# Kernel tuning notes

Measured on AMD Instinct MI355X. Metric: run time of the kernel, lower is better.

The kernel has to match this reference:

```python
import jax, jax.numpy as jnp
import numpy as np

B, N, D = 4, 4096, 1024
LN_EPS = 1e-5

def setup_inputs() -> dict:
    key = jax.random.key(0)
    ks = jax.random.split(key, 12)
    s = 1.0 / np.sqrt(D)
    return {
        "embeddings": jax.random.normal(ks[0], (B, N, D), dtype=jnp.float32),
        "edge_indices": jax.random.randint(ks[1], (2, 8192), 0, N, dtype=jnp.int64),
        "edge_times": jax.random.uniform(ks[2], (8192,), dtype=jnp.float32),
        "timestamps": jax.random.uniform(ks[3], (N,), dtype=jnp.float32),
        "Wq": jax.random.uniform(ks[4], (D, D), jnp.float32, -s, s),
        "bq": jax.random.uniform(ks[5], (D,), jnp.float32, -s, s),
        "Wk": jax.random.uniform(ks[6], (D, D), jnp.float32, -s, s),
        "bk": jax.random.uniform(ks[7], (D,), jnp.float32, -s, s),
        "Wv": jax.random.uniform(ks[8], (D, D), jnp.float32, -s, s),
        "bv": jax.random.uniform(ks[9], (D,), jnp.float32, -s, s),
        "gamma": jnp.ones((D,), jnp.float32),
        "beta": jnp.zeros((D,), jnp.float32),
    }

def reference(embeddings, edge_indices, edge_times, timestamps,
              Wq, bq, Wk, bk, Wv, bv, gamma, beta):
    # edge_indices / edge_times / timestamps are unused by the original forward.
    d = embeddings.shape[-1]
    q = jnp.einsum("bnd,ed->bne", embeddings, Wq) + bq   # [B,N,D]
    k = jnp.einsum("bnd,ed->bne", embeddings, Wk) + bk
    v = jnp.einsum("bnd,ed->bne", embeddings, Wv) + bv
    scores = jnp.einsum("bnd,bmd->bnm", q, k) / jnp.sqrt(jnp.asarray(d, embeddings.dtype))
    attn = jax.nn.softmax(scores, axis=-1)                # [B,N,N]
    attended = jnp.einsum("bnm,bmd->bnd", attn, v)
    x = embeddings + attended
    mu = jnp.mean(x, axis=-1, keepdims=True)
    var = jnp.mean(jnp.square(x - mu), axis=-1, keepdims=True)
    return gamma * (x - mu) * jax.lax.rsqrt(var + LN_EPS) + beta
```

## Files before the change

### kernel.cpp

```cpp
#include <hip/hip_runtime.h>
#include <hip/hip_fp8.h>

typedef unsigned short u16;
typedef unsigned char  u8;
typedef long long      i64;
using bf16x8 = __attribute__((ext_vector_type(8))) __bf16;
using f32x4  = __attribute__((ext_vector_type(4))) float;

__device__ __forceinline__ u16 f2bf(float f) {
    unsigned u = __builtin_bit_cast(unsigned, f);
    u += 0x7fffu + ((u >> 16) & 1u);
    return (u16)(u >> 16);
}
__device__ __forceinline__ float bf2f(u16 h) {
    unsigned u = ((unsigned)h) << 16;
    return __builtin_bit_cast(float, u);
}
__device__ __forceinline__ u8 f2fp8(float f) {
    __hip_fp8_e4m3 t(f);
    return t.__x;
}
__device__ __forceinline__ float wred_sum(float v) {
    #pragma unroll
    for (int o = 32; o; o >>= 1) v += __shfl_xor(v, o, 64);
    return v;
}

__device__ __forceinline__ void gl2lds16(const void* g, void* l) {
    __builtin_amdgcn_global_load_lds(
        (__attribute__((address_space(1))) void*)(g),
        (__attribute__((address_space(3))) void*)(l), 16, 0, 0);
}

__global__ __launch_bounds__(256)
void cast_bf16(const float* __restrict__ src, u16* __restrict__ dst, int n4) {
    int i = blockIdx.x * 256 + threadIdx.x;
    if (i < n4) {
        float4 f = ((const float4*)src)[i];
        ushort4 u;
        u.x = f2bf(f.x); u.y = f2bf(f.y); u.z = f2bf(f.z); u.w = f2bf(f.w);
        ((ushort4*)dst)[i] = u;
    }
}

template<int MODE>
__global__ __launch_bounds__(512, 2)
void gemm256(const u16* __restrict__ A, const u16* __restrict__ Bt,
             u16* __restrict__ oQ, u16* __restrict__ oK,
             const float* __restrict__ bQ, const float* __restrict__ bK,
             const float* __restrict__ bV,
             u8* __restrict__ oP, u8* __restrict__ oP2,
             float* __restrict__ sums, const float scale)
{
    __shared__ u16 smem[65536];
    const int tid = threadIdx.x;
    const int wv = tid >> 6, lane = tid & 63;
    const int wm = wv >> 2, wn = wv & 3;
    const int row0 = blockIdx.x << 8, col0 = blockIdx.y << 8;

    const size_t boff = (size_t)blockIdx.z * 4194304;
    const int srow = tid >> 2;
    const int scol = ((tid & 3) ^ ((tid >> 3) & 3)) << 3;
    const u16* gA = A + boff + (size_t)(row0 + srow) * 1024 + scol;
    const u16* gB = Bt + boff + (size_t)(col0 + srow) * 1024 + scol;
    char* lds = (char*)smem;
    const int wvo = wv << 10;

    const int fr = lane & 15, g = lane >> 4;
    const int kc = (g ^ ((fr >> 1) & 3)) << 4;

    f32x4 acc[8][4];
    #pragma unroll
    for (int i = 0; i < 8; i++)
        #pragma unroll
        for (int j = 0; j < 4; j++) acc[i][j] = (f32x4){0.f, 0.f, 0.f, 0.f};

    #define SG_A(ts, sl) { \
        gl2lds16(gA + (ts) * 32,          lds + (sl) * 32768 + wvo); \
        gl2lds16(gA + 131072 + (ts) * 32, lds + (sl) * 32768 + 8192 + wvo); }
    #define SG_B(ts, sl) { \
        gl2lds16(gB + (ts) * 32,          lds + (sl) * 32768 + 16384 + wvo); \
        gl2lds16(gB + 131072 + (ts) * 32, lds + (sl) * 32768 + 24576 + wvo); }

    SG_A(0, 0); SG_B(0, 0);
    SG_A(1, 1); SG_B(1, 1);
    SG_A(2, 2); SG_B(2, 2);
    asm volatile("s_waitcnt vmcnt(8)" ::: "memory");
    __builtin_amdgcn_s_barrier();

    for (int t = 0; t < 32; ++t) {
        const int slot = t & 3;
        const int ts = (t + 3) & 31;
        const int ns = (t + 3) & 3;
        const char* Ab = lds + slot * 32768;
        const char* Bb = Ab + 16384;

        SG_A(ts, ns);
        bf16x8 bf[4], af[4];
        #pragma unroll
        for (int j = 0; j < 4; ++j)
            bf[j] = *(const bf16x8*)(Bb + (wn * 64 + 16 * j + fr) * 64 + kc);
        #pragma unroll
        for (int i = 0; i < 4; ++i)
            af[i] = *(const bf16x8*)(Ab + (wm * 128 + 16 * i + fr) * 64 + kc);
        __builtin_amdgcn_sched_barrier(0);
        __builtin_amdgcn_s_barrier();
        asm volatile("s_waitcnt lgkmcnt(0)" ::: "memory");
        __builtin_amdgcn_sched_barrier(0);
        __builtin_amdgcn_s_setprio(1);
        #pragma unroll
        for (int i = 0; i < 4; ++i)
            #pragma unroll
            for (int j = 0; j < 4; ++j)
                acc[i][j] = __builtin_amdgcn_mfma_f32_16x16x32_bf16(af[i], bf[j], acc[i][j], 0, 0, 0);
        __builtin_amdgcn_s_setprio(0);

        SG_B(ts, ns);
        bf16x8 af2[4];
        #pragma unroll
        for (int i = 0; i < 4; ++i)
            af2[i] = *(const bf16x8*)(Ab + (wm * 128 + 64 + 16 * i + fr) * 64 + kc);
        asm volatile("s_waitcnt vmcnt(8)" ::: "memory");
        __builtin_amdgcn_sched_barrier(0);
        __builtin_amdgcn_s_barrier();
        asm volatile("s_waitcnt lgkmcnt(0)" ::: "memory");
        __builtin_amdgcn_sched_barrier(0);
        __builtin_amdgcn_s_setprio(1);
        #pragma unroll
        for (int i = 0; i < 4; ++i)
            #pragma unroll
            for (int j = 0; j < 4; ++j)
                acc[i + 4][j] = __builtin_amdgcn_mfma_f32_16x16x32_bf16(af2[i], bf[j], acc[i + 4][j], 0, 0, 0);
        __builtin_amdgcn_s_setprio(0);
    }
    #undef SG_A
    #undef SG_B

    asm volatile("s_waitcnt vmcnt(0)" ::: "memory");

    const int rB = (lane >> 4) << 2, cB = lane & 15;

    if (MODE == 0) {
        const int sel = col0 >> 10;
        if (sel < 2) {
            const float* bias = (sel == 0) ? bQ : bK;
            u16* dst = (sel == 0) ? oQ : oK;
            #pragma unroll
            for (int i = 0; i < 8; i++) {
                #pragma unroll
                for (int j = 0; j < 4; j++) {
                    const int m0 = row0 + wm * 128 + 16 * i + rB;
                    const int e  = (col0 & 1023) + wn * 64 + 16 * j + cB;
                    const float bb = bias[e];
                    #pragma unroll
                    for (int t = 0; t < 4; t++)
                        dst[(size_t)(m0 + t) * 1024 + e] = f2bf(acc[i][j][t] + bb);
                }
            }
        } else {
            const int b      = row0 >> 12;
            const int n_base = row0 & 4095;
            const int e0     = col0 & 1023;
            unsigned* lds32 = (unsigned*)smem;
            __syncthreads();
            #pragma unroll
            for (int i = 0; i < 8; i++) {
                const int n_l0 = wm * 128 + 16 * i + rB;
                const int gq   = n_l0 >> 4;
                const int kq   = (n_l0 >> 2) & 3;
                #pragma unroll
                for (int j = 0; j < 4; j++) {
                    const int e_p = wn * 64 + 16 * j + cB;
                    const float bb = bV[e0 + e_p];
                    union { u8 c[4]; unsigned u; } pk;
                    pk.c[0] = f2fp8(acc[i][j][0] + bb);
                    pk.c[1] = f2fp8(acc[i][j][1] + bb);
                    pk.c[2] = f2fp8(acc[i][j][2] + bb);
                    pk.c[3] = f2fp8(acc[i][j][3] + bb);
                    lds32[e_p * 64 + ((gq ^ (e_p & 15)) << 2) + kq] = pk.u;
                }
            }
            __syncthreads();
            #pragma unroll
            for (int it = 0; it < 8; ++it) {
                const int idx = it * 512 + tid;
                const int er  = idx >> 4;
                const int c16 = idx & 15;
                int4 v = *(const int4*)&lds32[er * 64 + ((c16 ^ (er & 15)) << 2)];
                *(int4*)&oP[(size_t)b * 4194304 +
                            (size_t)(e0 + er) * 4096 + n_base + c16 * 16] = v;
            }
        }
    } else {
        u8* Pz = blockIdx.z ? oP2 : oP;
        float* smz = sums + (blockIdx.z << 12);
        float psum[8][4];
        #pragma unroll
        for (int i = 0; i < 8; i++)
            #pragma unroll
            for (int t = 0; t < 4; t++) psum[i][t] = 0.f;

        #pragma unroll
        for (int i = 0; i < 8; i++) {
            const int m0 = row0 + wm * 128 + 16 * i + rB;
            #pragma unroll
            for (int j = 0; j < 4; j++) {
                const int c = col0 + wn * 64 + 16 * j + cB;
                #pragma unroll
                for (int t = 0; t < 4; t++) {
                    const float e = __expf(acc[i][j][t] * scale);
                    psum[i][t] += e;
                    Pz[(size_t)(m0 + t) * 4096 + c] = f2fp8(e);
                }
            }
        }
        #pragma unroll
        for (int i = 0; i < 8; i++) {
            #pragma unroll
            for (int t = 0; t < 4; t++) {
                float v = psum[i][t];
                v += __shfl_xor(v, 1, 64);
                v += __shfl_xor(v, 2, 64);
                v += __shfl_xor(v, 4, 64);
                v += __shfl_xor(v, 8, 64);
                if (cB == 0)
                    atomicAdd(&smz[row0 + wm * 128 + 16 * i + rB + t], v);
            }
        }
    }
}

__global__ __launch_bounds__(512, 2)
void pv256(const u8* __restrict__ p0, const u8* __restrict__ p1,
           const u8* __restrict__ p2, const u8* __restrict__ p3,
           const u8* __restrict__ vt8, const float* __restrict__ sums,
           float* __restrict__ out)
{
    __shared__ u8 smem[131072];
    const int b = blockIdx.z;
    const u8* Pb = (b == 0) ? p0 : (b == 1) ? p1 : (b == 2) ? p2 : p3;
    const u8* Vb = vt8 + (size_t)b * 4194304;
    const float* sm = sums + (b << 12);
    float* Ob = out + (size_t)b * 4194304;

    const int tid = threadIdx.x;
    const int wv = tid >> 6, lane = tid & 63;
    const int wm = wv >> 2, wn = wv & 3;
    const int row0 = blockIdx.x << 8, col0 = blockIdx.y << 8;

    const int srow = tid >> 2;
    const int sc16 = ((tid & 3) ^ ((tid >> 3) & 3)) << 4;
    const u8* gA = Pb + (size_t)(row0 + srow) * 4096 + sc16;
    const u8* gB = Vb + (size_t)(col0 + srow) * 4096 + sc16;
    char* lds = (char*)smem;
    const int wvo = wv << 10;

    const int fr = lane & 15, g = lane >> 4;
    const int sw = (fr >> 1) & 3;
    const int g2 = g >> 1, h8 = (g & 1) << 3;
    const int pc0 = ((g2 ^ sw) << 4) + h8;
    const int pc1 = (((2 + g2) ^ sw) << 4) + h8;

    f32x4 acc[8][4];
    #pragma unroll
    for (int i = 0; i < 8; i++)
        #pragma unroll
        for (int j = 0; j < 4; j++) acc[i][j] = (f32x4){0.f, 0.f, 0.f, 0.f};

    #define PG_A(ts, sl) { \
        gl2lds16(gA + (ts) * 64,          lds + (sl) * 32768 + wvo); \
        gl2lds16(gA + 524288 + (ts) * 64, lds + (sl) * 32768 + 8192 + wvo); }
    #define PG_B(ts, sl) { \
        gl2lds16(gB + (ts) * 64,          lds + (sl) * 32768 + 16384 + wvo); \
        gl2lds16(gB + 524288 + (ts) * 64, lds + (sl) * 32768 + 24576 + wvo); }

    PG_A(0, 0); PG_B(0, 0);
    PG_A(1, 1); PG_B(1, 1);
    PG_A(2, 2); PG_B(2, 2);
    asm volatile("s_waitcnt vmcnt(8)" ::: "memory");
    __builtin_amdgcn_s_barrier();

    for (int t = 0; t < 64; ++t) {
        const int slot = t & 3;
        const int ts = (t + 3) & 63;
        const int ns = (t + 3) & 3;
        const char* Ab = lds + slot * 32768;
        const char* Bb = Ab + 16384;

        PG_A(ts, ns);
        i64 af[8], bf[4];
        #pragma unroll
        for (int i = 0; i < 8; ++i) af[i] = *(const i64*)(Ab + (wm * 128 + 16 * i + fr) * 64 + pc0);
        #pragma unroll
        for (int j = 0; j < 4; ++j) bf[j] = *(const i64*)(Bb + (wn * 64 + 16 * j + fr) * 64 + pc0);
        __builtin_amdgcn_sched_barrier(0);
        __builtin_amdgcn_s_barrier();
        asm volatile("s_waitcnt lgkmcnt(0)" ::: "memory");
        __builtin_amdgcn_sched_barrier(0);
        __builtin_amdgcn_s_setprio(1);
        #pragma unroll
        for (int i = 0; i < 8; ++i)
            #pragma unroll
            for (int j = 0; j < 4; ++j)
                acc[i][j] = __builtin_amdgcn_mfma_f32_16x16x32_fp8_fp8(af[i], bf[j], acc[i][j], 0, 0, 0);
        __builtin_amdgcn_s_setprio(0);

        PG_B(ts, ns);
        #pragma unroll
        for (int i = 0; i < 8; ++i) af[i] = *(const i64*)(Ab + (wm * 128 + 16 * i + fr) * 64 + pc1);
        #pragma unroll
        for (int j = 0; j < 4; ++j) bf[j] = *(const i64*)(Bb + (wn * 64 + 16 * j + fr) * 64 + pc1);
        asm volatile("s_waitcnt vmcnt(8)" ::: "memory");
        __builtin_amdgcn_sched_barrier(0);
        __builtin_amdgcn_s_barrier();
        asm volatile("s_waitcnt lgkmcnt(0)" ::: "memory");
        __builtin_amdgcn_sched_barrier(0);
        __builtin_amdgcn_s_setprio(1);
        #pragma unroll
        for (int i = 0; i < 8; ++i)
            #pragma unroll
            for (int j = 0; j < 4; ++j)
                acc[i][j] = __builtin_amdgcn_mfma_f32_16x16x32_fp8_fp8(af[i], bf[j], acc[i][j], 0, 0, 0);
        __builtin_amdgcn_s_setprio(0);
    }
    #undef PG_A
    #undef PG_B

    asm volatile("s_waitcnt vmcnt(0)" ::: "memory");

    const int rB = (lane >> 4) << 2, cB = lane & 15;
    #pragma unroll
    for (int i = 0; i < 8; i++) {
        const int m0 = row0 + wm * 128 + 16 * i + rB;
        const float i0 = 1.0f / sm[m0];
        const float i1 = 1.0f / sm[m0 + 1];
        const float i2 = 1.0f / sm[m0 + 2];
        const float i3 = 1.0f / sm[m0 + 3];
        #pragma unroll
        for (int j = 0; j < 4; j++) {
            const int e = col0 + wn * 64 + 16 * j + cB;
            Ob[(size_t)(m0 + 0) * 1024 + e] = acc[i][j][0] * i0;
            Ob[(size_t)(m0 + 1) * 1024 + e] = acc[i][j][1] * i1;
            Ob[(size_t)(m0 + 2) * 1024 + e] = acc[i][j][2] * i2;
            Ob[(size_t)(m0 + 3) * 1024 + e] = acc[i][j][3] * i3;
        }
    }
}

__global__ __launch_bounds__(256)
void residual_ln(const float* __restrict__ emb, float* __restrict__ out,
                 const float* __restrict__ gamma, const float* __restrict__ beta) {
    const size_t row = blockIdx.x;
    const int t = threadIdx.x;
    const int wv = t >> 6, lane = t & 63;
    const size_t base = row * 1024 + t * 4;

    float4 ev = *(const float4*)(emb + base);
    float4 ov = *(const float4*)(out + base);
    float x0 = ev.x + ov.x, x1 = ev.y + ov.y, x2 = ev.z + ov.z, x3 = ev.w + ov.w;

    float s = x0 + x1 + x2 + x3;
    float q = x0 * x0 + x1 * x1 + x2 * x2 + x3 * x3;
    s = wred_sum(s);
    q = wred_sum(q);
    __shared__ float s1[4], s2[4];
    if (lane == 0) { s1[wv] = s; s2[wv] = q; }
    __syncthreads();
    s = s1[0] + s1[1] + s1[2] + s1[3];
    q = s2[0] + s2[1] + s2[2] + s2[3];

    const float mu  = s * (1.0f / 1024.0f);
    const float var = q * (1.0f / 1024.0f) - mu * mu;
    const float r   = rsqrtf(var + 1e-5f);

    float4 g  = *(const float4*)(gamma + t * 4);
    float4 be = *(const float4*)(beta + t * 4);
    float4 res;
    res.x = (x0 - mu) * r * g.x + be.x;
    res.y = (x1 - mu) * r * g.y + be.y;
    res.z = (x2 - mu) * r * g.z + be.z;
    res.w = (x3 - mu) * r * g.w + be.w;
    *(float4*)(out + base) = res;
}

extern "C" void kernel_launch(void* const* d_in, const int* in_sizes, int n_in,
                              void* d_out, int out_size, void* d_ws, size_t ws_size,
                              hipStream_t stream) {
    const float* emb   = (const float*)d_in[0];
    const float* Wq    = (const float*)d_in[4];
    const float* bq    = (const float*)d_in[5];
    const float* Wk    = (const float*)d_in[6];
    const float* bk    = (const float*)d_in[7];
    const float* Wv    = (const float*)d_in[8];
    const float* bv    = (const float*)d_in[9];
    const float* gamma = (const float*)d_in[10];
    const float* beta  = (const float*)d_in[11];
    float* out = (float*)d_out;

    char* ws = (char*)d_ws;
    if (ws_size < 140509184u) return;
    u16* Xbf = (u16*)(ws);
    u16* Wbf = (u16*)(ws + 33554432);
    u16* Qbf = (u16*)(ws + 39845888);
    u16* Kbf = (u16*)(ws + 73400320);

    u8*    P0   = (u8*)(ws);
    u8*    P1   = (u8*)(ws + 16777216);
    float* SUMS = (float*)(ws + 33554432);
    u8*    P3   = (u8*)(ws + 39845888);
    u8*    VT8  = (u8*)(ws + 106954752);
    u8*    P2   = (u8*)(ws + 123731968);

    cast_bf16<<<16384, 256, 0, stream>>>(emb, Xbf, 4194304);
    cast_bf16<<<1024, 256, 0, stream>>>(Wq, Wbf,           262144);
    cast_bf16<<<1024, 256, 0, stream>>>(Wk, Wbf + 1048576, 262144);
    cast_bf16<<<1024, 256, 0, stream>>>(Wv, Wbf + 2097152, 262144);

    gemm256<0><<<dim3(64, 12), 512, 0, stream>>>(Xbf, Wbf,
        Qbf, Kbf, bq, bk, bv, VT8, nullptr, nullptr, 1.0f);

    hipMemsetAsync(SUMS, 0, 65536, stream);

    gemm256<1><<<dim3(16, 16, 2), 512, 0, stream>>>(Qbf, Kbf,
        nullptr, nullptr, nullptr, nullptr, nullptr,
        P0, P1, SUMS, 0.03125f);
    gemm256<1><<<dim3(16, 16, 2), 512, 0, stream>>>(Qbf + 2 * 4194304, Kbf + 2 * 4194304,
        nullptr, nullptr, nullptr, nullptr, nullptr,
        P2, P3, SUMS + 8192, 0.03125f);

    pv256<<<dim3(16, 4, 4), 512, 0, stream>>>(P0, P1, P2, P3, VT8, SUMS, out);

    residual_ln<<<16384, 256, 0, stream>>>(emb, out, gamma, beta);
}
```

Measured before the change: 524.8 us.

## Use one barrier per k-step and interleave LDS reads with MFMA in GEMM loops

Both the bf16 projection GEMM and the fp8 PV GEMM main loops drop from two workgroup barriers per k-step to one. LDS fragment reads are split into halves with partial lgkmcnt waits so MFMAs on the first half can start while later reads are still in flight. The aim is to cut barrier stalls and LDS-latency exposure. The price is more live registers for the extra fragment arrays, and a risk of reading a stale or overwritten ring slot, since global-to-LDS prefetches are now issued before the consumer MFMAs without an intervening barrier.

```diff
diff --git a/kernel.cpp b/kernel.cpp
--- a/kernel.cpp
+++ b/kernel.cpp
@@ -31,6 +31,8 @@
         (__attribute__((address_space(1))) void*)(g),
         (__attribute__((address_space(3))) void*)(l), 16, 0, 0);
 }
+
+#define SBAR0() __builtin_amdgcn_sched_barrier(0)
 
 __global__ __launch_bounds__(256)
 void cast_bf16(const float* __restrict__ src, u16* __restrict__ dst, int n4) {
@@ -87,6 +89,7 @@
     SG_A(2, 2); SG_B(2, 2);
     asm volatile("s_waitcnt vmcnt(8)" ::: "memory");
     __builtin_amdgcn_s_barrier();
+    SBAR0();
 
     for (int t = 0; t < 32; ++t) {
         const int slot = t & 3;
@@ -95,43 +98,42 @@
         const char* Ab = lds + slot * 32768;
         const char* Bb = Ab + 16384;
 
-        SG_A(ts, ns);
-        bf16x8 bf[4], af[4];
+        bf16x8 bf[4], af[4], af2[4];
         #pragma unroll
         for (int j = 0; j < 4; ++j)
             bf[j] = *(const bf16x8*)(Bb + (wn * 64 + 16 * j + fr) * 64 + kc);
         #pragma unroll
         for (int i = 0; i < 4; ++i)
             af[i] = *(const bf16x8*)(Ab + (wm * 128 + 16 * i + fr) * 64 + kc);
-        __builtin_amdgcn_sched_barrier(0);
+        SBAR0();
+        SG_A(ts, ns);
+        #pragma unroll
+        for (int i = 0; i < 4; ++i)
+            af2[i] = *(const bf16x8*)(Ab + (wm * 128 + 64 + 16 * i + fr) * 64 + kc);
+        SG_B(ts, ns);
+        SBAR0();
+        asm volatile("s_waitcnt lgkmcnt(4)" ::: "memory");
+        SBAR0();
+        __builtin_amdgcn_s_setprio(1);
+        #pragma unroll
+        for (int i = 0; i < 4; ++i)
+            #pragma unroll
+            for (int j = 0; j < 4; ++j)
+                acc[i][j] = __builtin_amdgcn_mfma_f32_16x16x32_bf16(af[i], bf[j], acc[i][j], 0, 0, 0);
+        __builtin_amdgcn_s_setprio(0);
+        asm volatile("s_waitcnt lgkmcnt(0)" ::: "memory");
+        SBAR0();
+        __builtin_amdgcn_s_setprio(1);
+        #pragma unroll
+        for (int i = 0; i < 4; ++i)
+            #pragma unroll
+            for (int j = 0; j < 4; ++j)
+                acc[i + 4][j] = __builtin_amdgcn_mfma_f32_16x16x32_bf16(af2[i], bf[j], acc[i + 4][j], 0, 0, 0);
+        __builtin_amdgcn_s_setprio(0);
+        asm volatile("s_waitcnt vmcnt(8)" ::: "memory");
+        SBAR0();
         __builtin_amdgcn_s_barrier();
-        asm volatile("s_waitcnt lgkmcnt(0)" ::: "memory");
-        __builtin_amdgcn_sched_barrier(0);
-        __builtin_amdgcn_s_setprio(1);
-        #pragma unroll
-        for (int i = 0; i < 4; ++i)
-            #pragma unroll
-            for (int j = 0; j < 4; ++j)
-                acc[i][j] = __builtin_amdgcn_mfma_f32_16x16x32_bf16(af[i], bf[j], acc[i][j], 0, 0, 0);
-        __builtin_amdgcn_s_setprio(0);
-
-        SG_B(ts, ns);
-        bf16x8 af2[4];
-        #pragma unroll
-        for (int i = 0; i < 4; ++i)
-            af2[i] = *(const bf16x8*)(Ab + (wm * 128 + 64 + 16 * i + fr) * 64 + kc);
-        asm volatile("s_waitcnt vmcnt(8)" ::: "memory");
-        __builtin_amdgcn_sched_barrier(0);
-        __builtin_amdgcn_s_barrier();
-        asm volatile("s_waitcnt lgkmcnt(0)" ::: "memory");
-        __builtin_amdgcn_sched_barrier(0);
-        __builtin_amdgcn_s_setprio(1);
-        #pragma unroll
-        for (int i = 0; i < 4; ++i)
-            #pragma unroll
-            for (int j = 0; j < 4; ++j)
-                acc[i + 4][j] = __builtin_amdgcn_mfma_f32_16x16x32_bf16(af2[i], bf[j], acc[i + 4][j], 0, 0, 0);
-        __builtin_amdgcn_s_setprio(0);
+        SBAR0();
     }
     #undef SG_A
     #undef SG_B
@@ -279,6 +281,7 @@
     PG_A(2, 2); PG_B(2, 2);
     asm volatile("s_waitcnt vmcnt(8)" ::: "memory");
     __builtin_amdgcn_s_barrier();
+    SBAR0();
 
     for (int t = 0; t < 64; ++t) {
         const int slot = t & 3;
@@ -287,41 +290,65 @@
         const char* Ab = lds + slot * 32768;
         const char* Bb = Ab + 16384;
 
+        i64 af[8], bf[4], af2[8], bf2[4];
+        #pragma unroll
+        for (int j = 0; j < 4; ++j) bf[j] = *(const i64*)(Bb + (wn * 64 + 16 * j + fr) * 64 + pc0);
+        #pragma unroll
+        for (int i = 0; i < 4; ++i) af[i] = *(const i64*)(Ab + (wm * 128 + 16 * i + fr) * 64 + pc0);
+        SBAR0();
         PG_A(ts, ns);
-        i64 af[8], bf[4];
-        #pragma unroll
-        for (int i = 0; i < 8; ++i) af[i] = *(const i64*)(Ab + (wm * 128 + 16 * i + fr) * 64 + pc0);
-        #pragma unroll
-        for (int j = 0; j < 4; ++j) bf[j] = *(const i64*)(Bb + (wn * 64 + 16 * j + fr) * 64 + pc0);
-        __builtin_amdgcn_sched_barrier(0);
+        #pragma unroll
+        for (int i = 4; i < 8; ++i) af[i] = *(const i64*)(Ab + (wm * 128 + 16 * i + fr) * 64 + pc0);
+        SBAR0();
+        asm volatile("s_waitcnt lgkmcnt(4)" ::: "memory");
+        SBAR0();
+        __builtin_amdgcn_s_setprio(1);
+        #pragma unroll
+        for (int i = 0; i < 4; ++i)
+            #pragma unroll
+            for (int j = 0; j < 4; ++j)
+                acc[i][j] = __builtin_amdgcn_mfma_f32_16x16x32_fp8_fp8(af[i], bf[j], acc[i][j], 0, 0, 0);
+        __builtin_amdgcn_s_setprio(0);
+        PG_B(ts, ns);
+        #pragma unroll
+        for (int j = 0; j < 4; ++j) bf2[j] = *(const i64*)(Bb + (wn * 64 + 16 * j + fr) * 64 + pc1);
+        #pragma unroll
+        for (int i = 0; i < 4; ++i) af2[i] = *(const i64*)(Ab + (wm * 128 + 16 * i + fr) * 64 + pc1);
+        SBAR0();
+        asm volatile("s_waitcnt lgkmcnt(8)" ::: "memory");
+        SBAR0();
+        __builtin_amdgcn_s_setprio(1);
+        #pragma unroll
+        for (int i = 4; i < 8; ++i)
+            #pragma unroll
+            for (int j = 0; j < 4; ++j)
+                acc[i][j] = __builtin_amdgcn_mfma_f32_16x16x32_fp8_fp8(af[i], bf[j], acc[i][j], 0, 0, 0);
+        __builtin_amdgcn_s_setprio(0);
+        #pragma unroll
+        for (int i = 4; i < 8; ++i) af2[i] = *(const i64*)(Ab + (wm * 128 + 16 * i + fr) * 64 + pc1);
+        SBAR0();
+        asm volatile("s_waitcnt lgkmcnt(4)" ::: "memory");
+        SBAR0();
+        __builtin_amdgcn_s_setprio(1);
+        #pragma unroll
+        for (int i = 0; i < 4; ++i)
+            #pragma unroll
+            for (int j = 0; j < 4; ++j)
+                acc[i][j] = __builtin_amdgcn_mfma_f32_16x16x32_fp8_fp8(af2[i], bf2[j], acc[i][j], 0, 0, 0);
+        __builtin_amdgcn_s_setprio(0);
+        asm volatile("s_waitcnt lgkmcnt(0)" ::: "memory");
+        SBAR0();
+        __builtin_amdgcn_s_setprio(1);
+        #pragma unroll
+        for (int i = 4; i < 8; ++i)
+            #pragma unroll
+            for (int j = 0; j < 4; ++j)
+                acc[i][j] = __builtin_amdgcn_mfma_f32_16x16x32_fp8_fp8(af2[i], bf2[j], acc[i][j], 0, 0, 0);
+        __builtin_amdgcn_s_setprio(0);
+        asm volatile("s_waitcnt vmcnt(8)" ::: "memory");
+        SBAR0();
         __builtin_amdgcn_s_barrier();
-        asm volatile("s_waitcnt lgkmcnt(0)" ::: "memory");
-        __builtin_amdgcn_sched_barrier(0);
-        __builtin_amdgcn_s_setprio(1);
-        #pragma unroll
-        for (int i = 0; i < 8; ++i)
-            #pragma unroll
-            for (int j = 0; j < 4; ++j)
-                acc[i][j] = __builtin_amdgcn_mfma_f32_16x16x32_fp8_fp8(af[i], bf[j], acc[i][j], 0, 0, 0);
-        __builtin_amdgcn_s_setprio(0);
-
-        PG_B(ts, ns);
-        #pragma unroll
-        for (int i = 0; i < 8; ++i) af[i] = *(const i64*)(Ab + (wm * 128 + 16 * i + fr) * 64 + pc1);
-        #pragma unroll
-        for (int j = 0; j < 4; ++j) bf[j] = *(const i64*)(Bb + (wn * 64 + 16 * j + fr) * 64 + pc1);
-        asm volatile("s_waitcnt vmcnt(8)" ::: "memory");
-        __builtin_amdgcn_sched_barrier(0);
-        __builtin_amdgcn_s_barrier();
-        asm volatile("s_waitcnt lgkmcnt(0)" ::: "memory");
-        __builtin_amdgcn_sched_barrier(0);
-        __builtin_amdgcn_s_setprio(1);
-        #pragma unroll
-        for (int i = 0; i < 8; ++i)
-            #pragma unroll
-            for (int j = 0; j < 4; ++j)
-                acc[i][j] = __builtin_amdgcn_mfma_f32_16x16x32_fp8_fp8(af[i], bf[j], acc[i][j], 0, 0, 0);
-        __builtin_amdgcn_s_setprio(0);
+        SBAR0();
     }
     #undef PG_A
     #undef PG_B
```

Measured after the change: 567.8 us. +8.2%, slower.

## Permute fp8 P and V storage so PV GEMM loads 16-byte fragments

Applied to the files above, without the earlier changes.

Reorders the K dimension of the fp8 probability matrix and the transposed V tile when they are written, so each lane's two k-halves are contiguous. The PV GEMM can then fetch both halves with one 16-byte LDS read per fragment instead of two 8-byte reads, removing the second LDS load phase and its lgkmcnt wait. It also merges waits in the QKV GEMM and adds scheduling barriers. The cost is more index arithmetic in the epilogues and more live registers for the wider fragments.

```diff
diff --git a/kernel.cpp b/kernel.cpp
--- a/kernel.cpp
+++ b/kernel.cpp
@@ -6,6 +6,7 @@
 typedef long long      i64;
 using bf16x8 = __attribute__((ext_vector_type(8))) __bf16;
 using f32x4  = __attribute__((ext_vector_type(4))) float;
+using i64x2  = __attribute__((ext_vector_type(2))) long long;
 
 __device__ __forceinline__ u16 f2bf(float f) {
     unsigned u = __builtin_bit_cast(unsigned, f);
@@ -31,6 +32,8 @@
         (__attribute__((address_space(1))) void*)(g),
         (__attribute__((address_space(3))) void*)(l), 16, 0, 0);
 }
+
+#define SBAR0() __builtin_amdgcn_sched_barrier(0)
 
 __global__ __launch_bounds__(256)
 void cast_bf16(const float* __restrict__ src, u16* __restrict__ dst, int n4) {
@@ -87,6 +90,7 @@
     SG_A(2, 2); SG_B(2, 2);
     asm volatile("s_waitcnt vmcnt(8)" ::: "memory");
     __builtin_amdgcn_s_barrier();
+    SBAR0();
 
     for (int t = 0; t < 32; ++t) {
         const int slot = t & 3;
@@ -103,10 +107,10 @@
         #pragma unroll
         for (int i = 0; i < 4; ++i)
             af[i] = *(const bf16x8*)(Ab + (wm * 128 + 16 * i + fr) * 64 + kc);
-        __builtin_amdgcn_sched_barrier(0);
+        SBAR0();
         __builtin_amdgcn_s_barrier();
         asm volatile("s_waitcnt lgkmcnt(0)" ::: "memory");
-        __builtin_amdgcn_sched_barrier(0);
+        SBAR0();
         __builtin_amdgcn_s_setprio(1);
         #pragma unroll
         for (int i = 0; i < 4; ++i)
@@ -120,11 +124,10 @@
         #pragma unroll
         for (int i = 0; i < 4; ++i)
             af2[i] = *(const bf16x8*)(Ab + (wm * 128 + 64 + 16 * i + fr) * 64 + kc);
-        asm volatile("s_waitcnt vmcnt(8)" ::: "memory");
-        __builtin_amdgcn_sched_barrier(0);
+        asm volatile("s_waitcnt vmcnt(8) lgkmcnt(0)" ::: "memory");
+        SBAR0();
         __builtin_amdgcn_s_barrier();
-        asm volatile("s_waitcnt lgkmcnt(0)" ::: "memory");
-        __builtin_amdgcn_sched_barrier(0);
+        SBAR0();
         __builtin_amdgcn_s_setprio(1);
         #pragma unroll
         for (int i = 0; i < 4; ++i)
@@ -166,8 +169,12 @@
             #pragma unroll
             for (int i = 0; i < 8; i++) {
                 const int n_l0 = wm * 128 + 16 * i + rB;
-                const int gq   = n_l0 >> 4;
-                const int kq   = (n_l0 >> 2) & 3;
+                const int blk  = n_l0 >> 6;
+                const int q    = (n_l0 & 63) >> 2;
+                const int pd   = ((q >> 1) & 3) * 4 + ((q >> 3) << 1) + (q & 1);
+                const int dwi  = blk * 16 + pd;
+                const int G    = dwi >> 2;
+                const int kq   = dwi & 3;
                 #pragma unroll
                 for (int j = 0; j < 4; j++) {
                     const int e_p = wn * 64 + 16 * j + cB;
@@ -177,7 +184,7 @@
                     pk.c[1] = f2fp8(acc[i][j][1] + bb);
                     pk.c[2] = f2fp8(acc[i][j][2] + bb);
                     pk.c[3] = f2fp8(acc[i][j][3] + bb);
-                    lds32[e_p * 64 + ((gq ^ (e_p & 15)) << 2) + kq] = pk.u;
+                    lds32[e_p * 64 + ((G ^ (e_p & 15)) << 2) + kq] = pk.u;
                 }
             }
             __syncthreads();
@@ -205,7 +212,9 @@
             const int m0 = row0 + wm * 128 + 16 * i + rB;
             #pragma unroll
             for (int j = 0; j < 4; j++) {
-                const int c = col0 + wn * 64 + 16 * j + cB;
+                const int n64 = 16 * j + cB;
+                const int p   = ((n64 >> 3) & 3) * 16 + ((n64 >> 5) << 3) + (cB & 7);
+                const int c   = col0 + wn * 64 + p;
                 #pragma unroll
                 for (int t = 0; t < 4; t++) {
                     const float e = __expf(acc[i][j][t] * scale);
@@ -256,10 +265,7 @@
     const int wvo = wv << 10;
 
     const int fr = lane & 15, g = lane >> 4;
-    const int sw = (fr >> 1) & 3;
-    const int g2 = g >> 1, h8 = (g & 1) << 3;
-    const int pc0 = ((g2 ^ sw) << 4) + h8;
-    const int pc1 = (((2 + g2) ^ sw) << 4) + h8;
+    const int pc = ((g ^ ((fr >> 1) & 3)) << 4);
 
     f32x4 acc[8][4];
     #pragma unroll
@@ -279,6 +285,7 @@
     PG_A(2, 2); PG_B(2, 2);
     asm volatile("s_waitcnt vmcnt(8)" ::: "memory");
     __builtin_amdgcn_s_barrier();
+    SBAR0();
 
     for (int t = 0; t < 64; ++t) {
         const int slot = t & 3;
@@ -288,39 +295,36 @@
         const char* Bb = Ab + 16384;
 
         PG_A(ts, ns);
-        i64 af[8], bf[4];
-        #pragma unroll
-        for (int i = 0; i < 8; ++i) af[i] = *(const i64*)(Ab + (wm * 128 + 16 * i + fr) * 64 + pc0);
-        #pragma unroll
-        for (int j = 0; j < 4; ++j) bf[j] = *(const i64*)(Bb + (wn * 64 + 16 * j + fr) * 64 + pc0);
-        __builtin_amdgcn_sched_barrier(0);
+        i64x2 av[8], bv[4];
+        #pragma unroll
+        for (int j = 0; j < 4; ++j)
+            bv[j] = *(const i64x2*)(Bb + (wn * 64 + 16 * j + fr) * 64 + pc);
+        #pragma unroll
+        for (int i = 0; i < 8; ++i)
+            av[i] = *(const i64x2*)(Ab + (wm * 128 + 16 * i + fr) * 64 + pc);
+        SBAR0();
         __builtin_amdgcn_s_barrier();
         asm volatile("s_waitcnt lgkmcnt(0)" ::: "memory");
-        __builtin_amdgcn_sched_barrier(0);
+        SBAR0();
         __builtin_amdgcn_s_setprio(1);
         #pragma unroll
         for (int i = 0; i < 8; ++i)
             #pragma unroll
             for (int j = 0; j < 4; ++j)
-                acc[i][j] = __builtin_amdgcn_mfma_f32_16x16x32_fp8_fp8(af[i], bf[j], acc[i][j], 0, 0, 0);
+                acc[i][j] = __builtin_amdgcn_mfma_f32_16x16x32_fp8_fp8(av[i][0], bv[j][0], acc[i][j], 0, 0, 0);
         __builtin_amdgcn_s_setprio(0);
 
         PG_B(ts, ns);
-        #pragma unroll
-        for (int i = 0; i < 8; ++i) af[i] = *(const i64*)(Ab + (wm * 128 + 16 * i + fr) * 64 + pc1);
-        #pragma unroll
-        for (int j = 0; j < 4; ++j) bf[j] = *(const i64*)(Bb + (wn * 64 + 16 * j + fr) * 64 + pc1);
         asm volatile("s_waitcnt vmcnt(8)" ::: "memory");
-        __builtin_amdgcn_sched_barrier(0);
+        SBAR0();
         __builtin_amdgcn_s_barrier();
-        asm volatile("s_waitcnt lgkmcnt(0)" ::: "memory");
-        __builtin_amdgcn_sched_barrier(0);
+        SBAR0();
         __builtin_amdgcn_s_setprio(1);
         #pragma unroll
         for (int i = 0; i < 8; ++i)
             #pragma unroll
             for (int j = 0; j < 4; ++j)
-                acc[i][j] = __builtin_amdgcn_mfma_f32_16x16x32_fp8_fp8(af[i], bf[j], acc[i][j], 0, 0, 0);
+                acc[i][j] = __builtin_amdgcn_mfma_f32_16x16x32_fp8_fp8(av[i][1], bv[j][1], acc[i][j], 0, 0, 0);
         __builtin_amdgcn_s_setprio(0);
     }
     #undef PG_A
```

Measured after the change: 547.7 us. 4.4% more time.
